# Performance work log

Measured on AMD Instinct MI355X. Metric: run time of the kernel, lower is better.

The kernel has to match this reference:

```python
import jax, jax.numpy as jnp
import numpy as np

B, L, C = 4, 16384, 512   # batch, tokens (128x128 grid), dim
NH, WS = 8, 8             # num_heads, window grid (ws)
HD = C // NH              # head_dim = 64


def setup_inputs() -> dict:
    key = jax.random.key(0)
    k1, k2, k3, k4, k5 = jax.random.split(key, 5)
    return {
        "q":   jax.random.normal(k1, (B, L, C), dtype=jnp.float32),
        "kv":  jax.random.normal(k2, (B, L, C), dtype=jnp.float32),
        "Wq":  jax.random.normal(k3, (C, C), dtype=jnp.float32) * 0.02,
        "Wkv": jax.random.normal(k4, (C, 2 * C), dtype=jnp.float32) * 0.02,
        "Wfc": jax.random.normal(k5, (C, C), dtype=jnp.float32) * 0.02,
    }


def reference(q, kv, Wq, Wkv, Wfc):
    Bq, Lq, Cd = q.shape
    Lkv = kv.shape[1]
    nh, hd, ws = NH, Cd // NH, WS
    scale = hd ** (-0.5)
    hw_q = int(round(Lq ** 0.5))   # 128
    hw_k = int(round(Lkv ** 0.5))
    sq, sk = hw_q // ws, hw_k // ws  # window side lengths (16)

    qp = q @ Wq                                   # [B, Lq, C]
    kvp = (kv @ Wkv).reshape(Bq, Lkv, 2, Cd)
    k, v = kvp[:, :, 0], kvp[:, :, 1]             # [B, Lkv, C]

    def window(x, s):
        # [B, hw, hw, C] -> [B, ws*ws windows, heads, s*s tokens, hd]
        x = x.reshape(Bq, ws, s, ws, s, Cd).transpose(0, 1, 3, 2, 4, 5)
        x = x.reshape(Bq, ws * ws, s * s, nh, hd)
        return x.transpose(0, 1, 3, 2, 4)

    qw = window(qp, sq)   # [B, W, H, sq*sq, hd]
    kw = window(k, sk)    # [B, W, H, sk*sk, hd]
    vw = window(v, sk)

    attn = jnp.einsum('bwhqd,bwhkd->bwhqk', qw, kw) * scale
    attn = jax.nn.softmax(attn, axis=-1)
    o = jnp.einsum('bwhqk,bwhkd->bwhqd', attn, vw)  # [B, W, H, sq*sq, hd]

    # inverse window partition
    o = o.transpose(0, 1, 3, 2, 4).reshape(Bq, ws, ws, sq, sq, Cd)
    o = o.transpose(0, 1, 3, 2, 4, 5).reshape(Bq, Lq, Cd)
    return o @ Wfc
```

## Files before the change

### kernel.cpp

```cpp
#include <hip/hip_runtime.h>
#include <stdint.h>

#define BB 4
#define LL 16384
#define CC 512
#define MM (BB * LL)

typedef unsigned short u16;
typedef __bf16 bf16x8 __attribute__((ext_vector_type(8)));
typedef float f32x4 __attribute__((ext_vector_type(4)));
typedef u16 u16x8 __attribute__((ext_vector_type(8)));
typedef u16 u16x4 __attribute__((ext_vector_type(4)));

__device__ __forceinline__ u16 f2bf(float f) {
  return __builtin_bit_cast(u16, (__bf16)f);
}

__device__ __forceinline__ void gl_lds16(const void* g, void* l) {
  __builtin_amdgcn_global_load_lds((const __attribute__((address_space(1))) void*)g,
                                   (__attribute__((address_space(3))) void*)l,
                                   16, 0, 0);
}

__global__ __launch_bounds__(256) void prep_kernel(
    const float* __restrict__ q, const float* __restrict__ kv,
    const float* __restrict__ Wq, const float* __restrict__ Wkv,
    const float* __restrict__ Wfc, u16* __restrict__ qo, u16* __restrict__ kvo,
    u16* __restrict__ Wq_t, u16* __restrict__ Wkv_t, u16* __restrict__ Wfc_t) {
  __shared__ float tile[64][65];
  const int bid = blockIdx.x, tid = threadIdx.x;

  if (bid < 4096) {
    const int half = bid >> 11;
    const float* src = half ? kv : q;
    u16* dst = half ? kvo : qo;
    const int n16 = MM * CC / 16;
    const int stride = 2048 * 256;
    for (int i = (bid & 2047) * 256 + tid; i < n16; i += stride) {
      f32x4 a0 = reinterpret_cast<const f32x4*>(src)[4 * i + 0];
      f32x4 a1 = reinterpret_cast<const f32x4*>(src)[4 * i + 1];
      f32x4 a2 = reinterpret_cast<const f32x4*>(src)[4 * i + 2];
      f32x4 a3 = reinterpret_cast<const f32x4*>(src)[4 * i + 3];
      u16x8 o0, o1;
      o0[0] = f2bf(a0[0]); o0[1] = f2bf(a0[1]); o0[2] = f2bf(a0[2]); o0[3] = f2bf(a0[3]);
      o0[4] = f2bf(a1[0]); o0[5] = f2bf(a1[1]); o0[6] = f2bf(a1[2]); o0[7] = f2bf(a1[3]);
      o1[0] = f2bf(a2[0]); o1[1] = f2bf(a2[1]); o1[2] = f2bf(a2[2]); o1[3] = f2bf(a2[3]);
      o1[4] = f2bf(a3[0]); o1[5] = f2bf(a3[1]); o1[6] = f2bf(a3[2]); o1[7] = f2bf(a3[3]);
      reinterpret_cast<u16x8*>(dst)[2 * i + 0] = o0;
      reinterpret_cast<u16x8*>(dst)[2 * i + 1] = o1;
    }
    return;
  }

  const int wb = bid - 4096;
  const float* W; u16* Wt; int N, ti;
  if (wb < 64)       { W = Wq;  Wt = Wq_t;  N = 512;  ti = wb; }
  else if (wb < 192) { W = Wkv; Wt = Wkv_t; N = 1024; ti = wb - 64; }
  else               { W = Wfc; Wt = Wfc_t; N = 512;  ti = wb - 192; }
  const int ntn = N >> 6;
  const int kt = ti / ntn, nt = ti % ntn;
  const int k0 = kt << 6, n0 = nt << 6;
  {
    const int r = tid >> 4, c4 = tid & 15;
#pragma unroll
    for (int e = 0; e < 4; ++e) {
      int row = r + e * 16;
      f32x4 v = *reinterpret_cast<const f32x4*>(&W[(size_t)(k0 + row) * N + n0 + c4 * 4]);
      tile[row][c4 * 4 + 0] = v[0]; tile[row][c4 * 4 + 1] = v[1];
      tile[row][c4 * 4 + 2] = v[2]; tile[row][c4 * 4 + 3] = v[3];
    }
  }
  __syncthreads();
  {
    const int n = tid >> 2, qd = tid & 3;
#pragma unroll
    for (int e = 0; e < 2; ++e) {
      int c = qd * 2 + e;
      u16x8 o;
#pragma unroll
      for (int j = 0; j < 8; ++j) o[j] = f2bf(tile[c * 8 + j][n]);
      *reinterpret_cast<u16x8*>(&Wt[(size_t)(n0 + n) * 512 + k0 + c * 8]) = o;
    }
  }
}

template <bool OUT_F32>
__global__ __launch_bounds__(512, 2) void gemm256(const u16* __restrict__ A,
                                                  const u16* __restrict__ Bt,
                                                  void* __restrict__ Cp,
                                                  int M, int N, int K) {
  __shared__ __align__(16) u16 Al[2][16384];
  __shared__ __align__(16) u16 Bl[2][16384];
  const int nbn = N >> 8;
  const int nwg = gridDim.x;
  const int bid0 = blockIdx.x;
  const int cpx = nwg >> 3;
  const int bid = (bid0 & 7) * cpx + (bid0 >> 3);
  const int bm = bid / nbn, bn = bid % nbn;
  const size_t row0 = (size_t)bm << 8, col0 = (size_t)bn << 8;
  const int tid = threadIdx.x, lane = tid & 63;
  const int wv = tid >> 6, wm = wv >> 2, wn = wv & 3;
  const int ro = lane & 15, g4 = lane >> 4;
  const int NT = K >> 6;

  const int ci0 = tid, ci1 = tid + 512;
  const int r0 = ci0 >> 3, g0 = (ci0 & 7) ^ (r0 & 7);
  const int r1 = ci1 >> 3, g1 = (ci1 & 7) ^ (r1 & 7);

  auto stageA = [&](int half, int kt, u16* L) {
    gl_lds16(A + (row0 + half * 128 + r0) * (size_t)K + kt * 64 + g0 * 8, L + half * 8192 + ci0 * 8);
    gl_lds16(A + (row0 + half * 128 + r1) * (size_t)K + kt * 64 + g1 * 8, L + half * 8192 + ci1 * 8);
  };
  auto stageB = [&](int half, int kt, u16* L) {
    gl_lds16(Bt + (col0 + half * 128 + r0) * (size_t)K + kt * 64 + g0 * 8, L + half * 8192 + ci0 * 8);
    gl_lds16(Bt + (col0 + half * 128 + r1) * (size_t)K + kt * 64 + g1 * 8, L + half * 8192 + ci1 * 8);
  };

  const int aB = (wm * 128 + ro) * 64;
  const int bB = (wn * 64 + ro) * 64;
  const int sw0 = (g4 ^ (ro & 7)) * 8;
  const int sw1 = ((g4 + 4) ^ (ro & 7)) * 8;

  auto ldf = [&](const u16* p) { return *reinterpret_cast<const bf16x8*>(p); };

  f32x4 acc[8][4] = {};

  stageA(0, 0, Al[0]); stageA(1, 0, Al[0]); stageB(0, 0, Bl[0]); stageB(1, 0, Bl[0]);
  stageB(0, 1, Bl[1]); stageB(1, 1, Bl[1]);
  asm volatile("s_waitcnt vmcnt(4)" ::: "memory");
  __builtin_amdgcn_s_barrier();

  for (int t = 0; t < NT; t += 2) {
#pragma unroll
    for (int half = 0; half < 2; ++half) {
      const int u = t + half;
      u16* LA = Al[half];
      u16* LB = Bl[half];
      u16* LAn = Al[half ^ 1];
      const bool stA = (u + 1) < NT;
      const bool stB = (u + 2) < NT;
      bf16x8 bfr[4][2], af[2][2];

#pragma unroll
      for (int n = 0; n < 4; ++n) {
        bfr[n][0] = ldf(LB + bB + n * 1024 + sw0);
        bfr[n][1] = ldf(LB + bB + n * 1024 + sw1);
      }
      af[0][0] = ldf(LA + aB + sw0);        af[0][1] = ldf(LA + aB + sw1);
      af[1][0] = ldf(LA + aB + 1024 + sw0); af[1][1] = ldf(LA + aB + 1024 + sw1);
      if (stA) stageA(0, u + 1, LAn);
      __builtin_amdgcn_s_barrier();
      asm volatile("s_waitcnt lgkmcnt(0)" ::: "memory");
      __builtin_amdgcn_sched_barrier(0);
      __builtin_amdgcn_s_setprio(1);
#pragma unroll
      for (int m = 0; m < 2; ++m)
#pragma unroll
        for (int n = 0; n < 4; ++n) {
          acc[m][n] = __builtin_amdgcn_mfma_f32_16x16x32_bf16(af[m][0], bfr[n][0], acc[m][n], 0, 0, 0);
          acc[m][n] = __builtin_amdgcn_mfma_f32_16x16x32_bf16(af[m][1], bfr[n][1], acc[m][n], 0, 0, 0);
        }
      __builtin_amdgcn_s_setprio(0);
      __builtin_amdgcn_s_barrier();

#pragma unroll
      for (int ph = 1; ph < 4; ++ph) {
        af[0][0] = ldf(LA + aB + (2 * ph) * 1024 + sw0);
        af[0][1] = ldf(LA + aB + (2 * ph) * 1024 + sw1);
        af[1][0] = ldf(LA + aB + (2 * ph + 1) * 1024 + sw0);
        af[1][1] = ldf(LA + aB + (2 * ph + 1) * 1024 + sw1);
        if (ph == 1) { if (stA) stageA(1, u + 1, LAn); }
        else if (ph == 2) { if (stB) stageB(0, u + 2, LB); }
        else { if (stB) stageB(1, u + 2, LB); }
        __builtin_amdgcn_s_barrier();
        asm volatile("s_waitcnt lgkmcnt(0)" ::: "memory");
        __builtin_amdgcn_sched_barrier(0);
        __builtin_amdgcn_s_setprio(1);
#pragma unroll
        for (int m = 0; m < 2; ++m)
#pragma unroll
          for (int n = 0; n < 4; ++n) {
            acc[2 * ph + m][n] =
                __builtin_amdgcn_mfma_f32_16x16x32_bf16(af[m][0], bfr[n][0], acc[2 * ph + m][n], 0, 0, 0);
            acc[2 * ph + m][n] =
                __builtin_amdgcn_mfma_f32_16x16x32_bf16(af[m][1], bfr[n][1], acc[2 * ph + m][n], 0, 0, 0);
          }
        __builtin_amdgcn_s_setprio(0);
        if (ph == 3) {
          if (stB) asm volatile("s_waitcnt vmcnt(4)" ::: "memory");
          else     asm volatile("s_waitcnt vmcnt(0)" ::: "memory");
        }
        __builtin_amdgcn_s_barrier();
      }
    }
  }

#pragma unroll
  for (int m = 0; m < 8; ++m)
#pragma unroll
    for (int n = 0; n < 4; ++n)
#pragma unroll
      for (int j = 0; j < 4; ++j) {
        size_t r = row0 + wm * 128 + m * 16 + g4 * 4 + j;
        size_t c = col0 + wn * 64 + n * 16 + ro;
        if (OUT_F32)
          reinterpret_cast<float*>(Cp)[r * N + c] = acc[m][n][j];
        else
          reinterpret_cast<u16*>(Cp)[r * N + c] = f2bf(acc[m][n][j]);
      }
}

__global__ __launch_bounds__(512, 4) void attn_kernel(const u16* __restrict__ qp,
                                                      const u16* __restrict__ kvp,
                                                      u16* __restrict__ o) {
  __shared__ __align__(16) u16 Kl[256 * 64];
  __shared__ __align__(16) u16 Vt[64 * 256];
  __shared__ __align__(16) u16 Pl[8 * 1024];
  const int bid = blockIdx.x;
  const int h = bid & 7, w = (bid >> 3) & 63, b = bid >> 9;
  const int w1 = w >> 3, w2 = w & 7;
  const int tid = threadIdx.x, lane = tid & 63, wv = tid >> 6;

  auto lrow = [&](int t) { return (w1 * 16 + (t >> 4)) * 128 + w2 * 16 + (t & 15); };

#pragma unroll
  for (int p = 0; p < 4; ++p) {
    int ci = tid + p * 512;
    int r = ci >> 3, g = (ci & 7) ^ (r & 7);
    gl_lds16(kvp + ((size_t)(b * LL + lrow(r))) * 1024 + h * 64 + g * 8, Kl + ci * 8);
  }
  {
    const int tk = tid >> 1, half = tid & 1;
    const size_t base = ((size_t)(b * LL + lrow(tk))) * 1024 + 512 + h * 64 + half * 32;
#pragma unroll
    for (int c = 0; c < 4; ++c) {
      u16x8 vx = *reinterpret_cast<const u16x8*>(kvp + base + c * 8);
#pragma unroll
      for (int e = 0; e < 8; ++e) {
        int d = half * 32 + c * 8 + e;
        Vt[d * 256 + (((tk >> 3) ^ (d & 7)) * 8) + (tk & 7)] = vx[e];
      }
    }
  }
  __syncthreads();

  const int ro = lane & 15;
  const int g4 = lane >> 4;
  const float scale = 0.125f;
  const int swA = (g4 ^ (ro & 7)) * 8;
  const int swB = ((g4 + 4) ^ (ro & 7)) * 8;
  u16* PW = Pl + wv * 1024;

  auto ldf = [&](const u16* p) { return *reinterpret_cast<const bf16x8*>(p); };

#pragma unroll
  for (int rt = 0; rt < 2; ++rt) {
    const int tq = 32 * wv + 16 * rt + ro;
    const size_t qbase = ((size_t)(b * LL + lrow(tq))) * 512 + h * 64 + g4 * 8;
    const bf16x8 qf0 = *reinterpret_cast<const bf16x8*>(qp + qbase);
    const bf16x8 qf1 = *reinterpret_cast<const bf16x8*>(qp + qbase + 32);

    f32x4 sa[16] = {};
    __builtin_amdgcn_s_setprio(1);
#pragma unroll
    for (int ct = 0; ct < 16; ++ct) {
      bf16x8 kf0 = ldf(Kl + (16 * ct + ro) * 64 + swA);
      bf16x8 kf1 = ldf(Kl + (16 * ct + ro) * 64 + swB);
      sa[ct] = __builtin_amdgcn_mfma_f32_16x16x32_bf16(qf0, kf0, sa[ct], 0, 0, 0);
      sa[ct] = __builtin_amdgcn_mfma_f32_16x16x32_bf16(qf1, kf1, sa[ct], 0, 0, 0);
    }
    __builtin_amdgcn_s_setprio(0);

#pragma unroll
    for (int j = 0; j < 4; ++j) {
      float m = -1e30f;
#pragma unroll
      for (int ct = 0; ct < 16; ++ct) m = fmaxf(m, sa[ct][j]);
      m = fmaxf(m, __shfl_xor(m, 1));
      m = fmaxf(m, __shfl_xor(m, 2));
      m = fmaxf(m, __shfl_xor(m, 4));
      m = fmaxf(m, __shfl_xor(m, 8));
      m *= scale;
      float s = 0.f;
#pragma unroll
      for (int ct = 0; ct < 16; ++ct) {
        float p = __expf(sa[ct][j] * scale - m);
        sa[ct][j] = p;
        s += p;
      }
      s += __shfl_xor(s, 1);
      s += __shfl_xor(s, 2);
      s += __shfl_xor(s, 4);
      s += __shfl_xor(s, 8);
      float inv = 1.f / s;
#pragma unroll
      for (int ct = 0; ct < 16; ++ct) sa[ct][j] *= inv;
    }

    f32x4 oacc[4] = {};
#pragma unroll
    for (int kh = 0; kh < 4; ++kh) {
#pragma unroll
      for (int c = 0; c < 4; ++c)
#pragma unroll
        for (int j = 0; j < 4; ++j) {
          int rq = g4 * 4 + j;
          PW[rq * 64 + (((2 * c + (ro >> 3)) ^ (rq & 7)) * 8) + (ro & 7)] =
              f2bf(sa[kh * 4 + c][j]);
        }
      __builtin_amdgcn_s_setprio(1);
#pragma unroll
      for (int ks = 0; ks < 2; ++ks) {
        bf16x8 pf = ldf(PW + ro * 64 + (((ks * 4 + g4) ^ (ro & 7)) * 8));
        const int kkg = kh * 2 + ks;
#pragma unroll
        for (int cd = 0; cd < 4; ++cd) {
          bf16x8 vf = ldf(Vt + (16 * cd + ro) * 256 + (((kkg * 4 + g4) ^ (ro & 7)) * 8));
          oacc[cd] = __builtin_amdgcn_mfma_f32_16x16x32_bf16(pf, vf, oacc[cd], 0, 0, 0);
        }
      }
      __builtin_amdgcn_s_setprio(0);
    }

#pragma unroll
    for (int cd = 0; cd < 4; ++cd)
#pragma unroll
      for (int j = 0; j < 4; ++j) {
        int t = 32 * wv + 16 * rt + g4 * 4 + j;
        int d = 16 * cd + ro;
        o[((size_t)(b * LL + lrow(t))) * 512 + h * 64 + d] = f2bf(oacc[cd][j]);
      }
  }
}

extern "C" void kernel_launch(void* const* d_in, const int* in_sizes, int n_in,
                              void* d_out, int out_size, void* d_ws, size_t ws_size,
                              hipStream_t stream) {
  const float* q = (const float*)d_in[0];
  const float* kv = (const float*)d_in[1];
  const float* Wq = (const float*)d_in[2];
  const float* Wkv = (const float*)d_in[3];
  const float* Wfc = (const float*)d_in[4];
  float* out = (float*)d_out;
  char* ws = (char*)d_ws;

  u16* q_bf  = (u16*)(ws + 0);
  u16* kv_bf = (u16*)(ws + 67108864);
  u16* qp    = (u16*)(ws + 134217728);
  u16* kvp   = (u16*)(ws + 201326592);
  u16* Wq_t  = (u16*)(ws + 335544320);
  u16* Wkv_t = (u16*)(ws + 336068608);
  u16* Wfc_t = (u16*)(ws + 337117184);
  u16* o_buf = q_bf;

  prep_kernel<<<4352, 256, 0, stream>>>(q, kv, Wq, Wkv, Wfc, q_bf, kv_bf, Wq_t, Wkv_t, Wfc_t);

  gemm256<false><<<(MM / 256) * (CC / 256), 512, 0, stream>>>(q_bf, Wq_t, qp, MM, CC, CC);
  gemm256<false><<<(MM / 256) * (2 * CC / 256), 512, 0, stream>>>(kv_bf, Wkv_t, kvp, MM, 2 * CC, CC);

  attn_kernel<<<BB * 64 * 8, 512, 0, stream>>>(qp, kvp, o_buf);

  gemm256<true><<<(MM / 256) * (CC / 256), 512, 0, stream>>>(o_buf, Wfc_t, out, MM, CC, CC);
}
```

Measured before the change: 365.5 us.

## Triple-buffer A tiles in GEMM to prefetch two k-steps ahead

Grows the A shared-memory staging from two to three buffers, so A tiles are now fetched two k-iterations ahead, the same distance as B. The two-way unrolled loop becomes a single loop with rotating buffer pointers, and the wait counts are adjusted to keep 8 loads in flight. The aim is to hide more global-load latency behind the MFMA work. In exchange the block now uses 160 KB of LDS, which leaves no room for a second block per CU, and the rotating pointers may add address arithmetic.

```diff
diff --git a/kernel.cpp b/kernel.cpp
--- a/kernel.cpp
+++ b/kernel.cpp
@@ -89,7 +89,7 @@
                                                   const u16* __restrict__ Bt,
                                                   void* __restrict__ Cp,
                                                   int M, int N, int K) {
-  __shared__ __align__(16) u16 Al[2][16384];
+  __shared__ __align__(16) u16 Al[3][16384];
   __shared__ __align__(16) u16 Bl[2][16384];
   const int nbn = N >> 8;
   const int nwg = gridDim.x;
@@ -125,30 +125,50 @@
 
   f32x4 acc[8][4] = {};
 
-  stageA(0, 0, Al[0]); stageA(1, 0, Al[0]); stageB(0, 0, Bl[0]); stageB(1, 0, Bl[0]);
+  stageA(0, 0, Al[0]); stageA(1, 0, Al[0]);
+  stageB(0, 0, Bl[0]); stageB(1, 0, Bl[0]);
+  stageA(0, 1, Al[1]); stageA(1, 1, Al[1]);
   stageB(0, 1, Bl[1]); stageB(1, 1, Bl[1]);
-  asm volatile("s_waitcnt vmcnt(4)" ::: "memory");
+  asm volatile("s_waitcnt vmcnt(8)" ::: "memory");
   __builtin_amdgcn_s_barrier();
 
-  for (int t = 0; t < NT; t += 2) {
-#pragma unroll
-    for (int half = 0; half < 2; ++half) {
-      const int u = t + half;
-      u16* LA = Al[half];
-      u16* LB = Bl[half];
-      u16* LAn = Al[half ^ 1];
-      const bool stA = (u + 1) < NT;
-      const bool stB = (u + 2) < NT;
-      bf16x8 bfr[4][2], af[2][2];
-
+  u16* Acur = Al[0]; u16* Anxt = Al[1]; u16* Asta = Al[2];
+  u16* Bcur = Bl[0]; u16* Bnxt = Bl[1];
+
+  for (int u = 0; u < NT; ++u) {
+    const bool st = (u + 2) < NT;
+    bf16x8 bfr[4][2], af[2][2];
+
+#pragma unroll
+    for (int n = 0; n < 4; ++n) {
+      bfr[n][0] = ldf(Bcur + bB + n * 1024 + sw0);
+      bfr[n][1] = ldf(Bcur + bB + n * 1024 + sw1);
+    }
+    af[0][0] = ldf(Acur + aB + sw0);        af[0][1] = ldf(Acur + aB + sw1);
+    af[1][0] = ldf(Acur + aB + 1024 + sw0); af[1][1] = ldf(Acur + aB + 1024 + sw1);
+    if (st) stageA(0, u + 2, Asta);
+    __builtin_amdgcn_s_barrier();
+    asm volatile("s_waitcnt lgkmcnt(0)" ::: "memory");
+    __builtin_amdgcn_sched_barrier(0);
+    __builtin_amdgcn_s_setprio(1);
+#pragma unroll
+    for (int m = 0; m < 2; ++m)
 #pragma unroll
       for (int n = 0; n < 4; ++n) {
-        bfr[n][0] = ldf(LB + bB + n * 1024 + sw0);
-        bfr[n][1] = ldf(LB + bB + n * 1024 + sw1);
-      }
-      af[0][0] = ldf(LA + aB + sw0);        af[0][1] = ldf(LA + aB + sw1);
-      af[1][0] = ldf(LA + aB + 1024 + sw0); af[1][1] = ldf(LA + aB + 1024 + sw1);
-      if (stA) stageA(0, u + 1, LAn);
+        acc[m][n] = __builtin_amdgcn_mfma_f32_16x16x32_bf16(af[m][0], bfr[n][0], acc[m][n], 0, 0, 0);
+        acc[m][n] = __builtin_amdgcn_mfma_f32_16x16x32_bf16(af[m][1], bfr[n][1], acc[m][n], 0, 0, 0);
+      }
+    __builtin_amdgcn_s_setprio(0);
+    __builtin_amdgcn_s_barrier();
+
+#pragma unroll
+    for (int ph = 1; ph < 4; ++ph) {
+      af[0][0] = ldf(Acur + aB + (2 * ph) * 1024 + sw0);
+      af[0][1] = ldf(Acur + aB + (2 * ph) * 1024 + sw1);
+      af[1][0] = ldf(Acur + aB + (2 * ph + 1) * 1024 + sw0);
+      af[1][1] = ldf(Acur + aB + (2 * ph + 1) * 1024 + sw1);
+      if (ph == 1) { if (st) { stageA(1, u + 2, Asta); stageB(0, u + 2, Bcur); } }
+      else if (ph == 2) { if (st) stageB(1, u + 2, Bcur); }
       __builtin_amdgcn_s_barrier();
       asm volatile("s_waitcnt lgkmcnt(0)" ::: "memory");
       __builtin_amdgcn_sched_barrier(0);
@@ -157,42 +177,21 @@
       for (int m = 0; m < 2; ++m)
 #pragma unroll
         for (int n = 0; n < 4; ++n) {
-          acc[m][n] = __builtin_amdgcn_mfma_f32_16x16x32_bf16(af[m][0], bfr[n][0], acc[m][n], 0, 0, 0);
-          acc[m][n] = __builtin_amdgcn_mfma_f32_16x16x32_bf16(af[m][1], bfr[n][1], acc[m][n], 0, 0, 0);
+          acc[2 * ph + m][n] =
+              __builtin_amdgcn_mfma_f32_16x16x32_bf16(af[m][0], bfr[n][0], acc[2 * ph + m][n], 0, 0, 0);
+          acc[2 * ph + m][n] =
+              __builtin_amdgcn_mfma_f32_16x16x32_bf16(af[m][1], bfr[n][1], acc[2 * ph + m][n], 0, 0, 0);
         }
       __builtin_amdgcn_s_setprio(0);
+      if (ph == 3) {
+        if (st) asm volatile("s_waitcnt vmcnt(8)" ::: "memory");
+        else    asm volatile("s_waitcnt vmcnt(0)" ::: "memory");
+      }
       __builtin_amdgcn_s_barrier();
-
-#pragma unroll
-      for (int ph = 1; ph < 4; ++ph) {
-        af[0][0] = ldf(LA + aB + (2 * ph) * 1024 + sw0);
-        af[0][1] = ldf(LA + aB + (2 * ph) * 1024 + sw1);
-        af[1][0] = ldf(LA + aB + (2 * ph + 1) * 1024 + sw0);
-        af[1][1] = ldf(LA + aB + (2 * ph + 1) * 1024 + sw1);
-        if (ph == 1) { if (stA) stageA(1, u + 1, LAn); }
-        else if (ph == 2) { if (stB) stageB(0, u + 2, LB); }
-        else { if (stB) stageB(1, u + 2, LB); }
-        __builtin_amdgcn_s_barrier();
-        asm volatile("s_waitcnt lgkmcnt(0)" ::: "memory");
-        __builtin_amdgcn_sched_barrier(0);
-        __builtin_amdgcn_s_setprio(1);
-#pragma unroll
-        for (int m = 0; m < 2; ++m)
-#pragma unroll
-          for (int n = 0; n < 4; ++n) {
-            acc[2 * ph + m][n] =
-                __builtin_amdgcn_mfma_f32_16x16x32_bf16(af[m][0], bfr[n][0], acc[2 * ph + m][n], 0, 0, 0);
-            acc[2 * ph + m][n] =
-                __builtin_amdgcn_mfma_f32_16x16x32_bf16(af[m][1], bfr[n][1], acc[2 * ph + m][n], 0, 0, 0);
-          }
-        __builtin_amdgcn_s_setprio(0);
-        if (ph == 3) {
-          if (stB) asm volatile("s_waitcnt vmcnt(4)" ::: "memory");
-          else     asm volatile("s_waitcnt vmcnt(0)" ::: "memory");
-        }
-        __builtin_amdgcn_s_barrier();
-      }
-    }
+    }
+
+    u16* ta = Acur; Acur = Anxt; Anxt = Asta; Asta = ta;
+    u16* tb = Bcur; Bcur = Bnxt; Bnxt = tb;
   }
 
 #pragma unroll
```

New measurement: 356.3 us. 1.03x faster.

## Replace 256x256 GEMM tiles with 128x128 tiles and use nontemporal prep loads

Applied to the files above, without the earlier changes.

Rewrites the projection GEMMs to use 128x128 output tiles with 256 threads, K fixed at 512, a double-buffered A tile and a single-buffered B tile, targeting three workgroups per CU. More, smaller workgroups are meant to improve occupancy and load balance across CUs for these K=512 GEMMs. The trade-off is lower operand reuse per tile, which means more global traffic, plus a full vmcnt(0) drain every iteration. The fp32-to-bf16 conversion now uses nontemporal loads so the streamed inputs do not pollute the cache.

```diff
diff --git a/kernel.cpp b/kernel.cpp
--- a/kernel.cpp
+++ b/kernel.cpp
@@ -37,10 +37,11 @@
     const int n16 = MM * CC / 16;
     const int stride = 2048 * 256;
     for (int i = (bid & 2047) * 256 + tid; i < n16; i += stride) {
-      f32x4 a0 = reinterpret_cast<const f32x4*>(src)[4 * i + 0];
-      f32x4 a1 = reinterpret_cast<const f32x4*>(src)[4 * i + 1];
-      f32x4 a2 = reinterpret_cast<const f32x4*>(src)[4 * i + 2];
-      f32x4 a3 = reinterpret_cast<const f32x4*>(src)[4 * i + 3];
+      const f32x4* sp = reinterpret_cast<const f32x4*>(src) + 4 * i;
+      f32x4 a0 = __builtin_nontemporal_load(sp + 0);
+      f32x4 a1 = __builtin_nontemporal_load(sp + 1);
+      f32x4 a2 = __builtin_nontemporal_load(sp + 2);
+      f32x4 a3 = __builtin_nontemporal_load(sp + 3);
       u16x8 o0, o1;
       o0[0] = f2bf(a0[0]); o0[1] = f2bf(a0[1]); o0[2] = f2bf(a0[2]); o0[3] = f2bf(a0[3]);
       o0[4] = f2bf(a1[0]); o0[5] = f2bf(a1[1]); o0[6] = f2bf(a1[2]); o0[7] = f2bf(a1[3]);
@@ -85,123 +86,108 @@
 }
 
 template <bool OUT_F32>
-__global__ __launch_bounds__(512, 2) void gemm256(const u16* __restrict__ A,
+__global__ __launch_bounds__(256, 3) void gemm128(const u16* __restrict__ A,
                                                   const u16* __restrict__ Bt,
                                                   void* __restrict__ Cp,
-                                                  int M, int N, int K) {
-  __shared__ __align__(16) u16 Al[2][16384];
-  __shared__ __align__(16) u16 Bl[2][16384];
-  const int nbn = N >> 8;
+                                                  int N, int nbnl) {
+  constexpr int K = 512;
+  constexpr int NT = 8;
+  __shared__ __align__(16) u16 Al[2][8192];
+  __shared__ __align__(16) u16 Bl[8192];
   const int nwg = gridDim.x;
   const int bid0 = blockIdx.x;
   const int cpx = nwg >> 3;
   const int bid = (bid0 & 7) * cpx + (bid0 >> 3);
-  const int bm = bid / nbn, bn = bid % nbn;
-  const size_t row0 = (size_t)bm << 8, col0 = (size_t)bn << 8;
+  const int bm = bid >> nbnl, bn = bid & ((1 << nbnl) - 1);
+  const size_t row0 = (size_t)bm << 7, col0 = (size_t)bn << 7;
   const int tid = threadIdx.x, lane = tid & 63;
-  const int wv = tid >> 6, wm = wv >> 2, wn = wv & 3;
+  const int wv = tid >> 6, wm = wv >> 1, wn = wv & 1;
   const int ro = lane & 15, g4 = lane >> 4;
-  const int NT = K >> 6;
-
-  const int ci0 = tid, ci1 = tid + 512;
-  const int r0 = ci0 >> 3, g0 = (ci0 & 7) ^ (r0 & 7);
-  const int r1 = ci1 >> 3, g1 = (ci1 & 7) ^ (r1 & 7);
-
-  auto stageA = [&](int half, int kt, u16* L) {
-    gl_lds16(A + (row0 + half * 128 + r0) * (size_t)K + kt * 64 + g0 * 8, L + half * 8192 + ci0 * 8);
-    gl_lds16(A + (row0 + half * 128 + r1) * (size_t)K + kt * 64 + g1 * 8, L + half * 8192 + ci1 * 8);
+
+  auto stageA = [&](int kt, u16* L) {
+#pragma unroll
+    for (int c = 0; c < 4; ++c) {
+      int cc = tid + c * 256;
+      int r = cc >> 3, g = (cc & 7) ^ (r & 7);
+      gl_lds16(A + (row0 + r) * (size_t)K + kt * 64 + g * 8, L + cc * 8);
+    }
   };
-  auto stageB = [&](int half, int kt, u16* L) {
-    gl_lds16(Bt + (col0 + half * 128 + r0) * (size_t)K + kt * 64 + g0 * 8, L + half * 8192 + ci0 * 8);
-    gl_lds16(Bt + (col0 + half * 128 + r1) * (size_t)K + kt * 64 + g1 * 8, L + half * 8192 + ci1 * 8);
+  auto stageB = [&](int kt) {
+#pragma unroll
+    for (int c = 0; c < 4; ++c) {
+      int cc = tid + c * 256;
+      int r = cc >> 3, g = (cc & 7) ^ (r & 7);
+      gl_lds16(Bt + (col0 + r) * (size_t)K + kt * 64 + g * 8, Bl + cc * 8);
+    }
   };
 
-  const int aB = (wm * 128 + ro) * 64;
+  const int aB = (wm * 64 + ro) * 64;
   const int bB = (wn * 64 + ro) * 64;
   const int sw0 = (g4 ^ (ro & 7)) * 8;
   const int sw1 = ((g4 + 4) ^ (ro & 7)) * 8;
 
   auto ldf = [&](const u16* p) { return *reinterpret_cast<const bf16x8*>(p); };
 
-  f32x4 acc[8][4] = {};
-
-  stageA(0, 0, Al[0]); stageA(1, 0, Al[0]); stageB(0, 0, Bl[0]); stageB(1, 0, Bl[0]);
-  stageB(0, 1, Bl[1]); stageB(1, 1, Bl[1]);
-  asm volatile("s_waitcnt vmcnt(4)" ::: "memory");
+  f32x4 acc[4][4] = {};
+
+  stageA(0, Al[0]); stageB(0);
+  asm volatile("s_waitcnt vmcnt(0)" ::: "memory");
   __builtin_amdgcn_s_barrier();
 
-  for (int t = 0; t < NT; t += 2) {
-#pragma unroll
-    for (int half = 0; half < 2; ++half) {
-      const int u = t + half;
-      u16* LA = Al[half];
-      u16* LB = Bl[half];
-      u16* LAn = Al[half ^ 1];
-      const bool stA = (u + 1) < NT;
-      const bool stB = (u + 2) < NT;
-      bf16x8 bfr[4][2], af[2][2];
-
+  for (int u = 0; u < NT; ++u) {
+    u16* LA = Al[u & 1];
+    u16* LAn = Al[(u + 1) & 1];
+    const bool st = (u + 1) < NT;
+    bf16x8 bfr[4][2], af[2][2];
+
+#pragma unroll
+    for (int n = 0; n < 4; ++n) {
+      bfr[n][0] = ldf(Bl + bB + n * 1024 + sw0);
+      bfr[n][1] = ldf(Bl + bB + n * 1024 + sw1);
+    }
+    af[0][0] = ldf(LA + aB + sw0);        af[0][1] = ldf(LA + aB + sw1);
+    af[1][0] = ldf(LA + aB + 1024 + sw0); af[1][1] = ldf(LA + aB + 1024 + sw1);
+    if (st) stageA(u + 1, LAn);
+    __builtin_amdgcn_s_barrier();
+    asm volatile("s_waitcnt lgkmcnt(0)" ::: "memory");
+    __builtin_amdgcn_sched_barrier(0);
+    __builtin_amdgcn_s_setprio(1);
+#pragma unroll
+    for (int m = 0; m < 2; ++m)
 #pragma unroll
       for (int n = 0; n < 4; ++n) {
-        bfr[n][0] = ldf(LB + bB + n * 1024 + sw0);
-        bfr[n][1] = ldf(LB + bB + n * 1024 + sw1);
-      }
-      af[0][0] = ldf(LA + aB + sw0);        af[0][1] = ldf(LA + aB + sw1);
-      af[1][0] = ldf(LA + aB + 1024 + sw0); af[1][1] = ldf(LA + aB + 1024 + sw1);
-      if (stA) stageA(0, u + 1, LAn);
-      __builtin_amdgcn_s_barrier();
-      asm volatile("s_waitcnt lgkmcnt(0)" ::: "memory");
-      __builtin_amdgcn_sched_barrier(0);
-      __builtin_amdgcn_s_setprio(1);
-#pragma unroll
-      for (int m = 0; m < 2; ++m)
-#pragma unroll
-        for (int n = 0; n < 4; ++n) {
-          acc[m][n] = __builtin_amdgcn_mfma_f32_16x16x32_bf16(af[m][0], bfr[n][0], acc[m][n], 0, 0, 0);
-          acc[m][n] = __builtin_amdgcn_mfma_f32_16x16x32_bf16(af[m][1], bfr[n][1], acc[m][n], 0, 0, 0);
-        }
-      __builtin_amdgcn_s_setprio(0);
-      __builtin_amdgcn_s_barrier();
-
-#pragma unroll
-      for (int ph = 1; ph < 4; ++ph) {
-        af[0][0] = ldf(LA + aB + (2 * ph) * 1024 + sw0);
-        af[0][1] = ldf(LA + aB + (2 * ph) * 1024 + sw1);
-        af[1][0] = ldf(LA + aB + (2 * ph + 1) * 1024 + sw0);
-        af[1][1] = ldf(LA + aB + (2 * ph + 1) * 1024 + sw1);
-        if (ph == 1) { if (stA) stageA(1, u + 1, LAn); }
-        else if (ph == 2) { if (stB) stageB(0, u + 2, LB); }
-        else { if (stB) stageB(1, u + 2, LB); }
-        __builtin_amdgcn_s_barrier();
-        asm volatile("s_waitcnt lgkmcnt(0)" ::: "memory");
-        __builtin_amdgcn_sched_barrier(0);
-        __builtin_amdgcn_s_setprio(1);
-#pragma unroll
-        for (int m = 0; m < 2; ++m)
-#pragma unroll
-          for (int n = 0; n < 4; ++n) {
-            acc[2 * ph + m][n] =
-                __builtin_amdgcn_mfma_f32_16x16x32_bf16(af[m][0], bfr[n][0], acc[2 * ph + m][n], 0, 0, 0);
-            acc[2 * ph + m][n] =
-                __builtin_amdgcn_mfma_f32_16x16x32_bf16(af[m][1], bfr[n][1], acc[2 * ph + m][n], 0, 0, 0);
-          }
-        __builtin_amdgcn_s_setprio(0);
-        if (ph == 3) {
-          if (stB) asm volatile("s_waitcnt vmcnt(4)" ::: "memory");
-          else     asm volatile("s_waitcnt vmcnt(0)" ::: "memory");
-        }
-        __builtin_amdgcn_s_barrier();
-      }
-    }
-  }
-
-#pragma unroll
-  for (int m = 0; m < 8; ++m)
+        acc[m][n] = __builtin_amdgcn_mfma_f32_16x16x32_bf16(af[m][0], bfr[n][0], acc[m][n], 0, 0, 0);
+        acc[m][n] = __builtin_amdgcn_mfma_f32_16x16x32_bf16(af[m][1], bfr[n][1], acc[m][n], 0, 0, 0);
+      }
+    __builtin_amdgcn_s_setprio(0);
+    __builtin_amdgcn_s_barrier();
+
+    af[0][0] = ldf(LA + aB + 2048 + sw0); af[0][1] = ldf(LA + aB + 2048 + sw1);
+    af[1][0] = ldf(LA + aB + 3072 + sw0); af[1][1] = ldf(LA + aB + 3072 + sw1);
+    if (st) stageB(u + 1);
+    __builtin_amdgcn_s_barrier();
+    asm volatile("s_waitcnt lgkmcnt(0)" ::: "memory");
+    __builtin_amdgcn_sched_barrier(0);
+    __builtin_amdgcn_s_setprio(1);
+#pragma unroll
+    for (int m = 0; m < 2; ++m)
+#pragma unroll
+      for (int n = 0; n < 4; ++n) {
+        acc[2 + m][n] = __builtin_amdgcn_mfma_f32_16x16x32_bf16(af[m][0], bfr[n][0], acc[2 + m][n], 0, 0, 0);
+        acc[2 + m][n] = __builtin_amdgcn_mfma_f32_16x16x32_bf16(af[m][1], bfr[n][1], acc[2 + m][n], 0, 0, 0);
+      }
+    __builtin_amdgcn_s_setprio(0);
+    asm volatile("s_waitcnt vmcnt(0)" ::: "memory");
+    __builtin_amdgcn_s_barrier();
+  }
+
+#pragma unroll
+  for (int m = 0; m < 4; ++m)
 #pragma unroll
     for (int n = 0; n < 4; ++n)
 #pragma unroll
       for (int j = 0; j < 4; ++j) {
-        size_t r = row0 + wm * 128 + m * 16 + g4 * 4 + j;
+        size_t r = row0 + wm * 64 + m * 16 + g4 * 4 + j;
         size_t c = col0 + wn * 64 + n * 16 + ro;
         if (OUT_F32)
           reinterpret_cast<float*>(Cp)[r * N + c] = acc[m][n][j];
@@ -355,10 +341,10 @@
 
   prep_kernel<<<4352, 256, 0, stream>>>(q, kv, Wq, Wkv, Wfc, q_bf, kv_bf, Wq_t, Wkv_t, Wfc_t);
 
-  gemm256<false><<<(MM / 256) * (CC / 256), 512, 0, stream>>>(q_bf, Wq_t, qp, MM, CC, CC);
-  gemm256<false><<<(MM / 256) * (2 * CC / 256), 512, 0, stream>>>(kv_bf, Wkv_t, kvp, MM, 2 * CC, CC);
+  gemm128<false><<<2048, 256, 0, stream>>>(q_bf, Wq_t, qp, CC, 2);
+  gemm128<false><<<4096, 256, 0, stream>>>(kv_bf, Wkv_t, kvp, 2 * CC, 3);
 
   attn_kernel<<<BB * 64 * 8, 512, 0, stream>>>(qp, kvp, o_buf);
 
-  gemm256<true><<<(MM / 256) * (CC / 256), 512, 0, stream>>>(o_buf, Wfc_t, out, MM, CC, CC);
-}
+  gemm128<true><<<2048, 256, 0, stream>>>(o_buf, Wfc_t, out, CC, 2);
+}
```

New measurement: 366.7 us. About the same (+0.3%).
